# Kernel tuning notes

Measured on AMD Instinct MI355X. Metric: run time of the kernel, lower is better.

The kernel has to match this reference:

```python
import jax, jax.numpy as jnp
import numpy as np
import math

N_FEATURES = 64
GAMMA_ORDER = 0.5
ALPHA, BETA, ETA = 0.3, 0.4, 0.3
MAX_K = 50


def _make_coeffs():
    # gamma_values[0] = Gamma(g+1); gamma_values[m] (m>=1) = Gamma(m)*Gamma(g-m+2)
    g0 = math.gamma(GAMMA_ORDER + 1.0)
    coeffs = np.zeros(MAX_K + 1, dtype=np.float32)
    coeffs[0] = 1.0
    for k in range(1, MAX_K + 1):
        gv_k = math.gamma(k) * math.gamma(GAMMA_ORDER - k + 2.0)
        coeffs[k] = ((-1.0) ** k) * g0 / gv_k
    return jnp.asarray(coeffs)


def setup_inputs() -> dict:
    key = jax.random.key(0)
    k1, k2, k3, k4 = jax.random.split(key, 4)
    B, T, F = 4, 8192, N_FEATURES
    x = jax.random.normal(k1, (B, T, F), dtype=jnp.float32)
    weight_matrix = jax.random.normal(k2, (F, F), dtype=jnp.float32)
    bound = 1.0 / math.sqrt(F)
    proj_w = jax.random.uniform(k3, (F, F), dtype=jnp.float32, minval=-bound, maxval=bound)
    proj_b = jax.random.uniform(k4, (F,), dtype=jnp.float32, minval=-bound, maxval=bound)
    kappa = jnp.float32(0.1)
    coeffs = _make_coeffs()
    return {"x": x, "weight_matrix": weight_matrix, "proj_w": proj_w,
            "proj_b": proj_b, "kappa": kappa, "coeffs": coeffs}


def _fractional_derivative(x, coeffs):
    # causal conv: result[:, t, :] = sum_{k=0}^{min(t, max_k)} coeffs[k] * x[:, t-k, :]
    K = coeffs.shape[0]
    F = x.shape[-1]
    # depthwise 1D cross-correlation; kernel reversed so it implements x[t-k]
    kern = jnp.tile(coeffs[::-1][:, None, None], (1, 1, F))  # [K, 1, F]
    return jax.lax.conv_general_dilated(
        x, kern, window_strides=(1,), padding=[(K - 1, 0)],
        dimension_numbers=("NWC", "WIO", "NWC"), feature_group_count=F)


def reference(x, weight_matrix, proj_w, proj_b, kappa, coeffs):
    B, T, F = x.shape
    # 1) memory term: fractional derivative (causal conv)
    memory_term = _fractional_derivative(x, coeffs)

    # 2) coupling term: sum_j w[i,j] * tanh(x_i - x_j) * sigmoid(|x_i| + |x_j|)
    #    diagonal contributes tanh(0)=0, matching the i != j skip in the original.
    w = jax.nn.softmax(weight_matrix, axis=1)                 # [F, F]
    xi = x[..., :, None]                                      # [B, T, F, 1]
    xj = x[..., None, :]                                      # [B, T, 1, F]
    c = jnp.tanh(xi - xj) * jax.nn.sigmoid(jnp.abs(xi) + jnp.abs(xj))  # [B,T,F,F]
    coupling_term = jnp.einsum("btij,ij->bti", c, w)

    # 3) global term: proj(x[:, t]) * sum_{s=0}^{t} exp(-kappa * s)
    proj = x @ proj_w.T + proj_b                               # [B, T, F]
    kernel_cumsum = jnp.cumsum(jnp.exp(-kappa * jnp.arange(T, dtype=x.dtype)))
    global_term = proj * kernel_cumsum[None, :, None]

    output = ALPHA * memory_term + BETA * coupling_term + ETA * global_term
    return (output, memory_term)
```

## Files before the change

kernel.cpp:

```cpp
#include <hip/hip_runtime.h>
#include <hip/hip_fp16.h>
#include <math.h>

#define TT 8192
#define FF 64
#define TILE 32
#define HALO 50
#define ROWS (TILE + HALO)
#define XSTR 72

typedef float f32x2 __attribute__((ext_vector_type(2)));
typedef float f32x4 __attribute__((ext_vector_type(4)));
typedef _Float16 f16x8 __attribute__((ext_vector_type(8)));
typedef unsigned int u32x4 __attribute__((ext_vector_type(4)));
typedef unsigned int u32x2 __attribute__((ext_vector_type(2)));

__device__ __forceinline__ float rcpf(float x) { return __builtin_amdgcn_rcpf(x); }

__global__ void prep_kernel(const float* __restrict__ W, const float* __restrict__ PW,
                            __half* __restrict__ wsmH, u32x4* __restrict__ pwB) {
    const int lane = threadIdx.x;
    const int wv   = threadIdx.y;
    const int tid  = wv * 64 + lane;
    for (int it = 0; it < 16; ++it) {
        const int r = wv * 16 + it;
        float v = W[r * 64 + lane];
        float m = v;
        #pragma unroll
        for (int off = 32; off >= 1; off >>= 1)
            m = fmaxf(m, __shfl_xor(m, off, 64));
        float e = __expf(v - m);
        float s = e;
        #pragma unroll
        for (int off = 32; off >= 1; off >>= 1)
            s += __shfl_xor(s, off, 64);
        wsmH[lane * 64 + r] = __float2half(e * rcpf(s));
    }
    for (int s = tid; s < 512; s += 256) {
        const int n2 = s >> 6;
        const int ln = s & 63;
        const int i  = (n2 >> 1) * 16 + (ln & 15);
        const int k0 = (n2 & 1) * 32 + (ln >> 4) * 8;
        u32x4 frag;
        #pragma unroll
        for (int w = 0; w < 4; ++w) {
            const unsigned lo = __half_as_ushort(__float2half_rn(PW[i * 64 + k0 + 2 * w]));
            const unsigned hi = __half_as_ushort(__float2half_rn(PW[i * 64 + k0 + 2 * w + 1]));
            frag[w] = lo | (hi << 16);
        }
        pwB[s] = frag;
    }
}

__global__ __launch_bounds__(512, 8)
void mcao_main(const float* __restrict__ x,
               const __half* __restrict__ wsmH,
               const u32x4* __restrict__ pwB,
               const float* __restrict__ pb,
               const float* __restrict__ kap,
               const float* __restrict__ coeffs,
               float* __restrict__ out,
               float* __restrict__ memout) {
    __shared__ __align__(16) char smem[37408];
    __half* xsH = (__half*)smem;
    float*  P2  = (float*)smem;
    f32x2*  tuS = (f32x2*)(smem + 11808);
    __half* wS  = (__half*)(smem + 29216);

    const int tid  = threadIdx.x;
    const int lane = tid & 63;
    const int wv   = tid >> 6;

    const int sw = ((int)blockIdx.x & 7) * 128 + ((int)blockIdx.x >> 3);
    const int b  = sw >> 8;
    const int t0 = (sw & 255) * TILE;
    const float* xb = x + (size_t)b * TT * FF;

    for (int i4 = tid; i4 < ROWS * 16; i4 += 512) {
        const int s = i4 >> 4, f4 = i4 & 15, t = t0 - HALO + s;
        f32x4 v = {0.f, 0.f, 0.f, 0.f};
        if (t >= 0) v = *(const f32x4*)(xb + (size_t)t * 64 + f4 * 4);
        __half hv[4];
        #pragma unroll
        for (int q = 0; q < 4; ++q) hv[q] = __float2half_rn(v[q]);
        *(u32x2*)(&xsH[s * XSTR + f4 * 4]) = *(u32x2*)hv;
    }
    ((f32x4*)wS)[tid] = ((const f32x4*)wsmH)[tid];
    __syncthreads();

    float macc[4] = {0.f, 0.f, 0.f, 0.f};
    #pragma unroll
    for (int s = 0; s < 54; ++s) {
        const float xv = __half2float(xsH[(4 * wv + s) * XSTR + lane]);
        #pragma unroll
        for (int r = 0; r < 4; ++r) {
            const int k = r + 50 - s;
            if (0 <= k && k <= 50) macc[r] = fmaf(coeffs[k], xv, macc[r]);
        }
    }
    #pragma unroll
    for (int r = 0; r < 4; ++r)
        memout[(size_t)(b * TT + t0 + 4 * wv + r) * 64 + lane] = macc[r];

    const int mt = wv >> 2, nt = wv & 3;
    const int arow = HALO + mt * 16 + (lane & 15);
    const int kcol = (lane >> 4) * 8;
    f32x4 cfr = {0.f, 0.f, 0.f, 0.f};
    #pragma unroll
    for (int kt = 0; kt < 2; ++kt) {
        const f16x8 afr = *(const f16x8*)(&xsH[arow * XSTR + kt * 32 + kcol]);
        const f16x8 bfr = __builtin_bit_cast(f16x8, pwB[(nt * 2 + kt) * 64 + lane]);
        cfr = __builtin_amdgcn_mfma_f32_16x16x32_f16(afr, bfr, cfr, 0, 0, 0);
    }

    const int erow = tid >> 4, f0 = (tid & 15) * 4;
    __half hx[4];
    *(u32x2*)hx = *(const u32x2*)(&xsH[(HALO + erow) * XSTR + f0]);
    #pragma unroll
    for (int q = 0; q < 4; ++q) {
        const float xi = __half2float(hx[q]);
        f32x2 e;
        e.x = fmaf(-2.f, rcpf(__expf(2.f * xi) + 1.f), 1.f);
        e.y = __expf(-fabsf(xi));
        tuS[(f0 + q) * 34 + erow] = e;
    }
    __syncthreads();

    const int r  = lane & 31;
    const int h  = lane >> 5;
    const int ib = wv * 8 + h * 4;
    f32x2 tiP[2], uiP[2];
    #pragma unroll
    for (int q = 0; q < 4; ++q) {
        const f32x2 e = tuS[(ib + q) * 34 + r];
        tiP[q >> 1][q & 1] = e.x;
        uiP[q >> 1][q & 1] = e.y;
    }

    f32x2 cac0 = {0.f, 0.f}, cac1 = {0.f, 0.f};
    const f32x2 one2 = {1.f, 1.f};
    #pragma unroll 8
    for (int j = 0; j < 64; ++j) {
        const f32x2 e = tuS[j * 34 + r];
        __half wh[4];
        *(u32x2*)wh = *(const u32x2*)(&wS[j * 64 + ib]);
        const f32x2 tjj = {e.x, e.x}, ujj = {e.y, e.y};
        {
            const f32x2 d1  = __builtin_elementwise_fma(-tiP[0], tjj, one2);
            const f32x2 d2  = __builtin_elementwise_fma( uiP[0], ujj, one2);
            const f32x2 den = d1 * d2;
            f32x2 rr; rr.x = rcpf(den.x); rr.y = rcpf(den.y);
            const f32x2 s = (tiP[0] - tjj) * rr;
            cac0.x = fmaf(__half2float(wh[0]), s.x, cac0.x);
            cac0.y = fmaf(__half2float(wh[1]), s.y, cac0.y);
        }
        {
            const f32x2 d1  = __builtin_elementwise_fma(-tiP[1], tjj, one2);
            const f32x2 d2  = __builtin_elementwise_fma( uiP[1], ujj, one2);
            const f32x2 den = d1 * d2;
            f32x2 rr; rr.x = rcpf(den.x); rr.y = rcpf(den.y);
            const f32x2 s = (tiP[1] - tjj) * rr;
            cac1.x = fmaf(__half2float(wh[2]), s.x, cac1.x);
            cac1.y = fmaf(__half2float(wh[3]), s.y, cac1.y);
        }
    }

    {
        const int ic = nt * 16 + (lane & 15);
        const int rb = mt * 16 + (lane >> 4) * 4;
        #pragma unroll
        for (int reg = 0; reg < 4; ++reg)
            P2[ic * 33 + rb + reg] = cfr[reg];
    }
    __syncthreads();

    const float kappa = kap[0];
    const float ksum  = (1.f - __expf(-kappa * (float)(t0 + r + 1))) *
                        rcpf(1.f - __expf(-kappa));
    const f32x4 pbv = *(const f32x4*)(pb + ib);
    #pragma unroll
    for (int q = 0; q < 4; ++q) {
        const float cv = (q & 1) ? ((q >> 1) ? cac1.y : cac0.y)
                                 : ((q >> 1) ? cac1.x : cac0.x);
        const int idx = (ib + q) * 33 + r;
        P2[idx] = fmaf(0.4f, cv, 0.3f * (P2[idx] + pbv[q]) * ksum);
    }
    __syncthreads();

    #pragma unroll
    for (int rr2 = 0; rr2 < 4; ++rr2) {
        const int row = 4 * wv + rr2;
        out[(size_t)(b * TT + t0 + row) * 64 + lane] =
            fmaf(0.3f, macc[rr2], P2[lane * 33 + row]);
    }
}

extern "C" void kernel_launch(void* const* d_in, const int* in_sizes, int n_in,
                              void* d_out, int out_size, void* d_ws, size_t ws_size,
                              hipStream_t stream) {
    const float* x   = (const float*)d_in[0];
    const float* W   = (const float*)d_in[1];
    const float* PW  = (const float*)d_in[2];
    const float* pb  = (const float*)d_in[3];
    const float* kap = (const float*)d_in[4];
    const float* cf  = (const float*)d_in[5];

    float* out    = (float*)d_out;
    float* memout = out + (size_t)4 * TT * FF;

    __half* wsmH = (__half*)d_ws;
    u32x4*  pwB  = (u32x4*)((char*)d_ws + 8192);

    hipLaunchKernelGGL(prep_kernel, dim3(1), dim3(64, 4), 0, stream, W, PW, wsmH, pwB);
    hipLaunchKernelGGL(mcao_main, dim3(4 * (TT / TILE)), dim3(512), 0, stream,
                       x, wsmH, pwB, pb, kap, cf, out, memout);
}
```

Baseline: 45.23 us.

## Fuse FIR conv into coupling loop and compute tanh/exp terms during load

Interleaves the 54-tap causal convolution into the first 54 iterations of the 64-step coupling loop, using a zero-padded coefficient array built in the prep kernel so the branchless loop has no bounds checks. The tanh and exp(-|x|) values are computed from the fp32 loads during the staging phase, which removes one barrier and the fp16 readback. The aim is to overlap the convolution's FMAs and LDS reads with the rcp-heavy coupling math and to cut synchronization. In exchange, register pressure rises and the loop is split into two copies.

```diff
diff --git a/kernel.cpp b/kernel.cpp
--- a/kernel.cpp
+++ b/kernel.cpp
@@ -6,7 +6,7 @@
 #define FF 64
 #define TILE 32
 #define HALO 50
-#define ROWS (TILE + HALO)
+#define ROWS 82
 #define XSTR 72
 
 typedef float f32x2 __attribute__((ext_vector_type(2)));
@@ -18,7 +18,9 @@
 __device__ __forceinline__ float rcpf(float x) { return __builtin_amdgcn_rcpf(x); }
 
 __global__ void prep_kernel(const float* __restrict__ W, const float* __restrict__ PW,
-                            __half* __restrict__ wsmH, u32x4* __restrict__ pwB) {
+                            const float* __restrict__ C,
+                            __half* __restrict__ wsmH, u32x4* __restrict__ pwB,
+                            float* __restrict__ cpad) {
     const int lane = threadIdx.x;
     const int wv   = threadIdx.y;
     const int tid  = wv * 64 + lane;
@@ -50,22 +52,26 @@
         }
         pwB[s] = frag;
     }
+    if (tid < 57) {
+        const int k = tid - 3;
+        cpad[tid] = (k >= 0 && k <= 50) ? C[k] : 0.f;
+    }
 }
 
 __global__ __launch_bounds__(512, 8)
 void mcao_main(const float* __restrict__ x,
                const __half* __restrict__ wsmH,
                const u32x4* __restrict__ pwB,
+               const float* __restrict__ cpad,
                const float* __restrict__ pb,
                const float* __restrict__ kap,
-               const float* __restrict__ coeffs,
                float* __restrict__ out,
                float* __restrict__ memout) {
     __shared__ __align__(16) char smem[37408];
     __half* xsH = (__half*)smem;
     float*  P2  = (float*)smem;
     f32x2*  tuS = (f32x2*)(smem + 11808);
-    __half* wS  = (__half*)(smem + 29216);
+    __half* wT  = (__half*)(smem + 29216);
 
     const int tid  = threadIdx.x;
     const int lane = tid & 63;
@@ -84,86 +90,109 @@
         #pragma unroll
         for (int q = 0; q < 4; ++q) hv[q] = __float2half_rn(v[q]);
         *(u32x2*)(&xsH[s * XSTR + f4 * 4]) = *(u32x2*)hv;
-    }
-    ((f32x4*)wS)[tid] = ((const f32x4*)wsmH)[tid];
-    __syncthreads();
-
-    float macc[4] = {0.f, 0.f, 0.f, 0.f};
-    #pragma unroll
-    for (int s = 0; s < 54; ++s) {
-        const float xv = __half2float(xsH[(4 * wv + s) * XSTR + lane]);
-        #pragma unroll
-        for (int r = 0; r < 4; ++r) {
-            const int k = r + 50 - s;
-            if (0 <= k && k <= 50) macc[r] = fmaf(coeffs[k], xv, macc[r]);
-        }
-    }
-    #pragma unroll
-    for (int r = 0; r < 4; ++r)
-        memout[(size_t)(b * TT + t0 + 4 * wv + r) * 64 + lane] = macc[r];
+        if (s >= HALO) {
+            const int row = s - HALO;
+            #pragma unroll
+            for (int q = 0; q < 4; ++q) {
+                f32x2 e;
+                e.x = fmaf(-2.f, rcpf(__expf(2.f * v[q]) + 1.f), 1.f);
+                e.y = __expf(-fabsf(v[q]));
+                tuS[(f4 * 4 + q) * 34 + row] = e;
+            }
+        }
+    }
+    ((f32x4*)wT)[tid] = ((const f32x4*)wsmH)[tid];
+    __syncthreads();
 
     const int mt = wv >> 2, nt = wv & 3;
-    const int arow = HALO + mt * 16 + (lane & 15);
-    const int kcol = (lane >> 4) * 8;
+    const int marow = HALO + mt * 16 + (lane & 15);
+    const int kcol  = (lane >> 4) * 8;
     f32x4 cfr = {0.f, 0.f, 0.f, 0.f};
     #pragma unroll
     for (int kt = 0; kt < 2; ++kt) {
-        const f16x8 afr = *(const f16x8*)(&xsH[arow * XSTR + kt * 32 + kcol]);
+        const f16x8 afr = *(const f16x8*)(&xsH[marow * XSTR + kt * 32 + kcol]);
         const f16x8 bfr = __builtin_bit_cast(f16x8, pwB[(nt * 2 + kt) * 64 + lane]);
         cfr = __builtin_amdgcn_mfma_f32_16x16x32_f16(afr, bfr, cfr, 0, 0, 0);
     }
-
-    const int erow = tid >> 4, f0 = (tid & 15) * 4;
-    __half hx[4];
-    *(u32x2*)hx = *(const u32x2*)(&xsH[(HALO + erow) * XSTR + f0]);
-    #pragma unroll
-    for (int q = 0; q < 4; ++q) {
-        const float xi = __half2float(hx[q]);
-        f32x2 e;
-        e.x = fmaf(-2.f, rcpf(__expf(2.f * xi) + 1.f), 1.f);
-        e.y = __expf(-fabsf(xi));
-        tuS[(f0 + q) * 34 + erow] = e;
-    }
-    __syncthreads();
 
     const int r  = lane & 31;
     const int h  = lane >> 5;
     const int ib = wv * 8 + h * 4;
-    f32x2 tiP[2], uiP[2];
-    #pragma unroll
-    for (int q = 0; q < 4; ++q) {
-        const f32x2 e = tuS[(ib + q) * 34 + r];
-        tiP[q >> 1][q & 1] = e.x;
-        uiP[q >> 1][q & 1] = e.y;
-    }
-
+    f32x2 tiP0, tiP1, uiP0, uiP1;
+    {
+        const f32x2 e0 = tuS[(ib + 0) * 34 + r];
+        const f32x2 e1 = tuS[(ib + 1) * 34 + r];
+        const f32x2 e2 = tuS[(ib + 2) * 34 + r];
+        const f32x2 e3 = tuS[(ib + 3) * 34 + r];
+        tiP0.x = e0.x; tiP0.y = e1.x; uiP0.x = e0.y; uiP0.y = e1.y;
+        tiP1.x = e2.x; tiP1.y = e3.x; uiP1.x = e2.y; uiP1.y = e3.y;
+    }
+
+    float macc[4] = {0.f, 0.f, 0.f, 0.f};
     f32x2 cac0 = {0.f, 0.f}, cac1 = {0.f, 0.f};
     const f32x2 one2 = {1.f, 1.f};
-    #pragma unroll 8
-    for (int j = 0; j < 64; ++j) {
-        const f32x2 e = tuS[j * 34 + r];
+    const int firrow = 4 * wv;
+
+    #pragma unroll 4
+    for (int m = 0; m < 54; ++m) {
+        const f32x2 e = tuS[m * 34 + r];
         __half wh[4];
-        *(u32x2*)wh = *(const u32x2*)(&wS[j * 64 + ib]);
+        *(u32x2*)wh = *(const u32x2*)(&wT[m * 64 + ib]);
+        const float xv = __half2float(xsH[(firrow + m) * XSTR + lane]);
+        #pragma unroll
+        for (int r2 = 0; r2 < 4; ++r2)
+            macc[r2] = fmaf(cpad[r2 + 53 - m], xv, macc[r2]);
         const f32x2 tjj = {e.x, e.x}, ujj = {e.y, e.y};
         {
-            const f32x2 d1  = __builtin_elementwise_fma(-tiP[0], tjj, one2);
-            const f32x2 d2  = __builtin_elementwise_fma( uiP[0], ujj, one2);
-            const f32x2 den = d1 * d2;
-            f32x2 rr; rr.x = rcpf(den.x); rr.y = rcpf(den.y);
-            const f32x2 s = (tiP[0] - tjj) * rr;
+            const f32x2 d1  = __builtin_elementwise_fma(-tiP0, tjj, one2);
+            const f32x2 d2  = __builtin_elementwise_fma( uiP0, ujj, one2);
+            const f32x2 den = d1 * d2;
+            f32x2 rr; rr.x = rcpf(den.x); rr.y = rcpf(den.y);
+            const f32x2 s = (tiP0 - tjj) * rr;
             cac0.x = fmaf(__half2float(wh[0]), s.x, cac0.x);
             cac0.y = fmaf(__half2float(wh[1]), s.y, cac0.y);
         }
         {
-            const f32x2 d1  = __builtin_elementwise_fma(-tiP[1], tjj, one2);
-            const f32x2 d2  = __builtin_elementwise_fma( uiP[1], ujj, one2);
-            const f32x2 den = d1 * d2;
-            f32x2 rr; rr.x = rcpf(den.x); rr.y = rcpf(den.y);
-            const f32x2 s = (tiP[1] - tjj) * rr;
+            const f32x2 d1  = __builtin_elementwise_fma(-tiP1, tjj, one2);
+            const f32x2 d2  = __builtin_elementwise_fma( uiP1, ujj, one2);
+            const f32x2 den = d1 * d2;
+            f32x2 rr; rr.x = rcpf(den.x); rr.y = rcpf(den.y);
+            const f32x2 s = (tiP1 - tjj) * rr;
             cac1.x = fmaf(__half2float(wh[2]), s.x, cac1.x);
             cac1.y = fmaf(__half2float(wh[3]), s.y, cac1.y);
         }
     }
+    #pragma unroll 4
+    for (int m = 54; m < 64; ++m) {
+        const f32x2 e = tuS[m * 34 + r];
+        __half wh[4];
+        *(u32x2*)wh = *(const u32x2*)(&wT[m * 64 + ib]);
+        const f32x2 tjj = {e.x, e.x}, ujj = {e.y, e.y};
+        {
+            const f32x2 d1  = __builtin_elementwise_fma(-tiP0, tjj, one2);
+            const f32x2 d2  = __builtin_elementwise_fma( uiP0, ujj, one2);
+            const f32x2 den = d1 * d2;
+            f32x2 rr; rr.x = rcpf(den.x); rr.y = rcpf(den.y);
+            const f32x2 s = (tiP0 - tjj) * rr;
+            cac0.x = fmaf(__half2float(wh[0]), s.x, cac0.x);
+            cac0.y = fmaf(__half2float(wh[1]), s.y, cac0.y);
+        }
+        {
+            const f32x2 d1  = __builtin_elementwise_fma(-tiP1, tjj, one2);
+            const f32x2 d2  = __builtin_elementwise_fma( uiP1, ujj, one2);
+            const f32x2 den = d1 * d2;
+            f32x2 rr; rr.x = rcpf(den.x); rr.y = rcpf(den.y);
+            const f32x2 s = (tiP1 - tjj) * rr;
+            cac1.x = fmaf(__half2float(wh[2]), s.x, cac1.x);
+            cac1.y = fmaf(__half2float(wh[3]), s.y, cac1.y);
+        }
+    }
+
+    #pragma unroll
+    for (int r2 = 0; r2 < 4; ++r2)
+        memout[(size_t)(b * TT + t0 + firrow + r2) * 64 + lane] = macc[r2];
+
+    __syncthreads();
 
     {
         const int ic = nt * 16 + (lane & 15);
@@ -210,8 +239,10 @@
 
     __half* wsmH = (__half*)d_ws;
     u32x4*  pwB  = (u32x4*)((char*)d_ws + 8192);
-
-    hipLaunchKernelGGL(prep_kernel, dim3(1), dim3(64, 4), 0, stream, W, PW, wsmH, pwB);
+    float*  cpad = (float*)((char*)d_ws + 16384);
+
+    hipLaunchKernelGGL(prep_kernel, dim3(1), dim3(64, 4), 0, stream,
+                       W, PW, cf, wsmH, pwB, cpad);
     hipLaunchKernelGGL(mcao_main, dim3(4 * (TT / TILE)), dim3(512), 0, stream,
-                       x, wsmH, pwB, pb, kap, cf, out, memout);
+                       x, wsmH, pwB, cpad, pb, kap, out, memout);
 }
```

New measurement: 45.78 us. No clear change (+1.2%).

## Double time tile to 64 rows and fuse FIR into coupling loop

Applied to the files above, without the earlier changes.

Doubles the time tile per block to 64 rows, which halves the grid and cuts the share of loaded halo rows. Each wave now handles 8 output rows and 8 features, and the causal FIR accumulation is interleaved into the 64-iteration coupling loop using a zero-padded coefficient array built in the prep kernel. The tanh and exp terms are computed straight from the fp32 load, and each wave issues two MFMA tiles. The cost is more shared memory and registers per block, with launch bounds lowered to 4 blocks per SM.

```diff
diff --git a/kernel.cpp b/kernel.cpp
--- a/kernel.cpp
+++ b/kernel.cpp
@@ -4,9 +4,9 @@
 
 #define TT 8192
 #define FF 64
-#define TILE 32
+#define TILE 64
 #define HALO 50
-#define ROWS (TILE + HALO)
+#define ROWS 114
 #define XSTR 72
 
 typedef float f32x2 __attribute__((ext_vector_type(2)));
@@ -18,7 +18,9 @@
 __device__ __forceinline__ float rcpf(float x) { return __builtin_amdgcn_rcpf(x); }
 
 __global__ void prep_kernel(const float* __restrict__ W, const float* __restrict__ PW,
-                            __half* __restrict__ wsmH, u32x4* __restrict__ pwB) {
+                            const float* __restrict__ C,
+                            __half* __restrict__ wsmH, u32x4* __restrict__ pwB,
+                            float* __restrict__ cpad2) {
     const int lane = threadIdx.x;
     const int wv   = threadIdx.y;
     const int tid  = wv * 64 + lane;
@@ -50,30 +52,34 @@
         }
         pwB[s] = frag;
     }
+    if (tid < 65) {
+        const int k = tid - 7;
+        cpad2[tid] = (k >= 0 && k <= 50) ? C[k] : 0.f;
+    }
 }
 
-__global__ __launch_bounds__(512, 8)
+__global__ __launch_bounds__(512, 4)
 void mcao_main(const float* __restrict__ x,
                const __half* __restrict__ wsmH,
                const u32x4* __restrict__ pwB,
+               const float* __restrict__ cpad2,
                const float* __restrict__ pb,
                const float* __restrict__ kap,
-               const float* __restrict__ coeffs,
                float* __restrict__ out,
                float* __restrict__ memout) {
-    __shared__ __align__(16) char smem[37408];
+    __shared__ __align__(16) char smem[57888];
     __half* xsH = (__half*)smem;
-    float*  P2  = (float*)smem;
-    f32x2*  tuS = (f32x2*)(smem + 11808);
-    __half* wS  = (__half*)(smem + 29216);
+    f32x2*  tuS = (f32x2*)(smem + 16416);
+    float*  P2  = (float*)(smem + 16416);
+    __half* wT  = (__half*)(smem + 49696);
 
     const int tid  = threadIdx.x;
     const int lane = tid & 63;
     const int wv   = tid >> 6;
 
-    const int sw = ((int)blockIdx.x & 7) * 128 + ((int)blockIdx.x >> 3);
-    const int b  = sw >> 8;
-    const int t0 = (sw & 255) * TILE;
+    const int sw = ((int)blockIdx.x & 7) * 64 + ((int)blockIdx.x >> 3);
+    const int b  = sw >> 7;
+    const int t0 = (sw & 127) * TILE;
     const float* xb = x + (size_t)b * TT * FF;
 
     for (int i4 = tid; i4 < ROWS * 16; i4 += 512) {
@@ -84,114 +90,107 @@
         #pragma unroll
         for (int q = 0; q < 4; ++q) hv[q] = __float2half_rn(v[q]);
         *(u32x2*)(&xsH[s * XSTR + f4 * 4]) = *(u32x2*)hv;
-    }
-    ((f32x4*)wS)[tid] = ((const f32x4*)wsmH)[tid];
-    __syncthreads();
-
-    float macc[4] = {0.f, 0.f, 0.f, 0.f};
-    #pragma unroll
-    for (int s = 0; s < 54; ++s) {
-        const float xv = __half2float(xsH[(4 * wv + s) * XSTR + lane]);
-        #pragma unroll
-        for (int r = 0; r < 4; ++r) {
-            const int k = r + 50 - s;
-            if (0 <= k && k <= 50) macc[r] = fmaf(coeffs[k], xv, macc[r]);
-        }
-    }
-    #pragma unroll
-    for (int r = 0; r < 4; ++r)
-        memout[(size_t)(b * TT + t0 + 4 * wv + r) * 64 + lane] = macc[r];
-
-    const int mt = wv >> 2, nt = wv & 3;
-    const int arow = HALO + mt * 16 + (lane & 15);
-    const int kcol = (lane >> 4) * 8;
-    f32x4 cfr = {0.f, 0.f, 0.f, 0.f};
-    #pragma unroll
-    for (int kt = 0; kt < 2; ++kt) {
-        const f16x8 afr = *(const f16x8*)(&xsH[arow * XSTR + kt * 32 + kcol]);
-        const f16x8 bfr = __builtin_bit_cast(f16x8, pwB[(nt * 2 + kt) * 64 + lane]);
-        cfr = __builtin_amdgcn_mfma_f32_16x16x32_f16(afr, bfr, cfr, 0, 0, 0);
-    }
-
-    const int erow = tid >> 4, f0 = (tid & 15) * 4;
-    __half hx[4];
-    *(u32x2*)hx = *(const u32x2*)(&xsH[(HALO + erow) * XSTR + f0]);
-    #pragma unroll
-    for (int q = 0; q < 4; ++q) {
-        const float xi = __half2float(hx[q]);
-        f32x2 e;
-        e.x = fmaf(-2.f, rcpf(__expf(2.f * xi) + 1.f), 1.f);
-        e.y = __expf(-fabsf(xi));
-        tuS[(f0 + q) * 34 + erow] = e;
-    }
-    __syncthreads();
-
-    const int r  = lane & 31;
-    const int h  = lane >> 5;
-    const int ib = wv * 8 + h * 4;
-    f32x2 tiP[2], uiP[2];
-    #pragma unroll
-    for (int q = 0; q < 4; ++q) {
-        const f32x2 e = tuS[(ib + q) * 34 + r];
+        if (s >= HALO) {
+            const int row = s - HALO;
+            #pragma unroll
+            for (int q = 0; q < 4; ++q) {
+                f32x2 e;
+                e.x = fmaf(-2.f, rcpf(__expf(2.f * v[q]) + 1.f), 1.f);
+                e.y = __expf(-fabsf(v[q]));
+                tuS[(f4 * 4 + q) * 65 + row] = e;
+            }
+        }
+    }
+    ((f32x4*)wT)[tid] = ((const f32x4*)wsmH)[tid];
+    __syncthreads();
+
+    const int mt = wv >> 1;
+    const int marow = HALO + mt * 16 + (lane & 15);
+    const int kcol  = (lane >> 4) * 8;
+    f32x4 cfr[2] = {{0.f,0.f,0.f,0.f}, {0.f,0.f,0.f,0.f}};
+    #pragma unroll
+    for (int tb = 0; tb < 2; ++tb) {
+        const int nt = (wv & 1) * 2 + tb;
+        #pragma unroll
+        for (int kt = 0; kt < 2; ++kt) {
+            const f16x8 afr = *(const f16x8*)(&xsH[marow * XSTR + kt * 32 + kcol]);
+            const f16x8 bfr = __builtin_bit_cast(f16x8, pwB[(nt * 2 + kt) * 64 + lane]);
+            cfr[tb] = __builtin_amdgcn_mfma_f32_16x16x32_f16(afr, bfr, cfr[tb], 0, 0, 0);
+        }
+    }
+
+    const int r  = lane;
+    const int ib = wv * 8;
+    f32x2 tiP[4], uiP[4];
+    #pragma unroll
+    for (int q = 0; q < 8; ++q) {
+        const f32x2 e = tuS[(ib + q) * 65 + r];
         tiP[q >> 1][q & 1] = e.x;
         uiP[q >> 1][q & 1] = e.y;
     }
 
-    f32x2 cac0 = {0.f, 0.f}, cac1 = {0.f, 0.f};
+    float macc[8] = {0,0,0,0,0,0,0,0};
+    f32x2 cac[4] = {{0,0},{0,0},{0,0},{0,0}};
     const f32x2 one2 = {1.f, 1.f};
-    #pragma unroll 8
-    for (int j = 0; j < 64; ++j) {
-        const f32x2 e = tuS[j * 34 + r];
-        __half wh[4];
-        *(u32x2*)wh = *(const u32x2*)(&wS[j * 64 + ib]);
+    const int firrow = 8 * wv;
+
+    #pragma unroll
+    for (int m = 0; m < 64; ++m) {
+        const f32x2 e = tuS[m * 65 + r];
+        __half wh[8];
+        *(u32x4*)wh = *(const u32x4*)(&wT[m * 64 + ib]);
+        if (m < 58) {
+            const float xv = __half2float(xsH[(firrow + m) * XSTR + lane]);
+            #pragma unroll
+            for (int r2 = 0; r2 < 8; ++r2)
+                macc[r2] = fmaf(cpad2[r2 + 57 - m], xv, macc[r2]);
+        }
         const f32x2 tjj = {e.x, e.x}, ujj = {e.y, e.y};
-        {
-            const f32x2 d1  = __builtin_elementwise_fma(-tiP[0], tjj, one2);
-            const f32x2 d2  = __builtin_elementwise_fma( uiP[0], ujj, one2);
+        #pragma unroll
+        for (int g = 0; g < 4; ++g) {
+            const f32x2 d1  = __builtin_elementwise_fma(-tiP[g], tjj, one2);
+            const f32x2 d2  = __builtin_elementwise_fma( uiP[g], ujj, one2);
             const f32x2 den = d1 * d2;
             f32x2 rr; rr.x = rcpf(den.x); rr.y = rcpf(den.y);
-            const f32x2 s = (tiP[0] - tjj) * rr;
-            cac0.x = fmaf(__half2float(wh[0]), s.x, cac0.x);
-            cac0.y = fmaf(__half2float(wh[1]), s.y, cac0.y);
-        }
-        {
-            const f32x2 d1  = __builtin_elementwise_fma(-tiP[1], tjj, one2);
-            const f32x2 d2  = __builtin_elementwise_fma( uiP[1], ujj, one2);
-            const f32x2 den = d1 * d2;
-            f32x2 rr; rr.x = rcpf(den.x); rr.y = rcpf(den.y);
-            const f32x2 s = (tiP[1] - tjj) * rr;
-            cac1.x = fmaf(__half2float(wh[2]), s.x, cac1.x);
-            cac1.y = fmaf(__half2float(wh[3]), s.y, cac1.y);
-        }
-    }
-
-    {
+            const f32x2 s = (tiP[g] - tjj) * rr;
+            cac[g].x = fmaf(__half2float(wh[2*g]),   s.x, cac[g].x);
+            cac[g].y = fmaf(__half2float(wh[2*g+1]), s.y, cac[g].y);
+        }
+    }
+
+    #pragma unroll
+    for (int r2 = 0; r2 < 8; ++r2)
+        memout[(size_t)(b * TT + t0 + firrow + r2) * 64 + lane] = macc[r2];
+
+    __syncthreads();
+
+    #pragma unroll
+    for (int tb = 0; tb < 2; ++tb) {
+        const int nt = (wv & 1) * 2 + tb;
         const int ic = nt * 16 + (lane & 15);
         const int rb = mt * 16 + (lane >> 4) * 4;
         #pragma unroll
         for (int reg = 0; reg < 4; ++reg)
-            P2[ic * 33 + rb + reg] = cfr[reg];
+            P2[ic * 65 + rb + reg] = cfr[tb][reg];
     }
     __syncthreads();
 
     const float kappa = kap[0];
     const float ksum  = (1.f - __expf(-kappa * (float)(t0 + r + 1))) *
                         rcpf(1.f - __expf(-kappa));
-    const f32x4 pbv = *(const f32x4*)(pb + ib);
-    #pragma unroll
-    for (int q = 0; q < 4; ++q) {
-        const float cv = (q & 1) ? ((q >> 1) ? cac1.y : cac0.y)
-                                 : ((q >> 1) ? cac1.x : cac0.x);
-        const int idx = (ib + q) * 33 + r;
-        P2[idx] = fmaf(0.4f, cv, 0.3f * (P2[idx] + pbv[q]) * ksum);
-    }
-    __syncthreads();
-
-    #pragma unroll
-    for (int rr2 = 0; rr2 < 4; ++rr2) {
-        const int row = 4 * wv + rr2;
+    #pragma unroll
+    for (int q = 0; q < 8; ++q) {
+        const float cv  = (q & 1) ? cac[q >> 1].y : cac[q >> 1].x;
+        const int   idx = (ib + q) * 65 + r;
+        P2[idx] = fmaf(0.4f, cv, 0.3f * (P2[idx] + pb[ib + q]) * ksum);
+    }
+    __syncthreads();
+
+    #pragma unroll
+    for (int rr2 = 0; rr2 < 8; ++rr2) {
+        const int row = firrow + rr2;
         out[(size_t)(b * TT + t0 + row) * 64 + lane] =
-            fmaf(0.3f, macc[rr2], P2[lane * 33 + row]);
+            fmaf(0.3f, macc[rr2], P2[lane * 65 + row]);
     }
 }
 
@@ -208,10 +207,12 @@
     float* out    = (float*)d_out;
     float* memout = out + (size_t)4 * TT * FF;
 
-    __half* wsmH = (__half*)d_ws;
-    u32x4*  pwB  = (u32x4*)((char*)d_ws + 8192);
-
-    hipLaunchKernelGGL(prep_kernel, dim3(1), dim3(64, 4), 0, stream, W, PW, wsmH, pwB);
+    __half* wsmH  = (__half*)d_ws;
+    u32x4*  pwB   = (u32x4*)((char*)d_ws + 8192);
+    float*  cpad2 = (float*)((char*)d_ws + 16384);
+
+    hipLaunchKernelGGL(prep_kernel, dim3(1), dim3(64, 4), 0, stream,
+                       W, PW, cf, wsmH, pwB, cpad2);
     hipLaunchKernelGGL(mcao_main, dim3(4 * (TT / TILE)), dim3(512), 0, stream,
-                       x, wsmH, pwB, pb, kap, cf, out, memout);
+                       x, wsmH, pwB, cpad2, pb, kap, out, memout);
 }
```

Result: faster. 43.90 us (-2.9%).
